# Performance work log

Hardware: AMD Instinct MI355X
Metric: run time of the kernel (lower is better)

## Reference

```python
import math
import jax, jax.numpy as jnp
import numpy as np

B, S, D_MODEL, H = 2, 2048, 1024, 16
D_HEAD = D_MODEL // H
NEG = -90000000000.0


def setup_inputs() -> dict:
    key = jax.random.key(0)
    ks = jax.random.split(key, 12)
    scale = 1.0 / math.sqrt(D_MODEL)
    return {
        "Q": jax.random.normal(ks[0], (B, S, D_MODEL), jnp.float32),
        "K": jax.random.normal(ks[1], (B, S, D_MODEL), jnp.float32),
        "V": jax.random.normal(ks[2], (B, S, D_MODEL), jnp.float32),
        "mask": jax.random.randint(ks[3], (B, 1, S, S), 0, 2).astype(bool),
        "Wq": jax.random.normal(ks[4], (D_MODEL, D_MODEL), jnp.float32) * scale,
        "bq": jnp.zeros((D_MODEL,), jnp.float32),
        "Wk": jax.random.normal(ks[5], (D_MODEL, D_MODEL), jnp.float32) * scale,
        "bk": jnp.zeros((D_MODEL,), jnp.float32),
        "Wv": jax.random.normal(ks[6], (D_MODEL, D_MODEL), jnp.float32) * scale,
        "bv": jnp.zeros((D_MODEL,), jnp.float32),
        "Wo": jax.random.normal(ks[7], (D_MODEL, D_MODEL), jnp.float32) * scale,
        "bo": jnp.zeros((D_MODEL,), jnp.float32),
    }


def _split_heads(x):
    # (B, S, D) -> (B, H, S, Dh)
    b, s, _ = x.shape
    return x.reshape(b, s, H, D_HEAD).transpose(0, 2, 1, 3)


def reference(Q, K, V, mask, Wq, bq, Wk, bk, Wv, bv, Wo, bo):
    q = _split_heads(Q @ Wq.T + bq)
    k = _split_heads(K @ Wk.T + bk)
    v = _split_heads(V @ Wv.T + bv)
    # scaled dot product with additive mask (mask.float() * -9e10)
    scores = jnp.einsum("bhqd,bhkd->bhqk", q, k) / math.sqrt(D_HEAD)
    scores = scores + mask.astype(scores.dtype) * NEG
    attn = jax.nn.softmax(scores, axis=-1)
    ctx = jnp.einsum("bhqk,bhkd->bhqd", attn, v)  # (B, H, S, Dh)
    ctx = ctx.transpose(0, 2, 1, 3).reshape(Q.shape[0], q.shape[2], D_MODEL)
    return ctx @ Wo.T + bo
```

## Files before the change

### kernel.cpp

```cpp
#include <hip/hip_runtime.h>
#include <hip/hip_bf16.h>


typedef __bf16 bf16x8 __attribute__((ext_vector_type(8)));
typedef float f32x4 __attribute__((ext_vector_type(4)));

#define S_LEN 2048
#define DM 1024
#define NH 16
#define DH 64
#define MROWS 4096

static __device__ __forceinline__ unsigned short f2bf(float f) {
    __hip_bfloat16 h = __float2bfloat16(f);
    unsigned short u; __builtin_memcpy(&u, &h, 2); return u;
}

static __device__ __forceinline__ bf16x8 cvt8(float4 a, float4 b) {
    bf16x8 o;
    o[0] = (__bf16)a.x; o[1] = (__bf16)a.y; o[2] = (__bf16)a.z; o[3] = (__bf16)a.w;
    o[4] = (__bf16)b.x; o[5] = (__bf16)b.y; o[6] = (__bf16)b.z; o[7] = (__bf16)b.w;
    return o;
}

__global__ __launch_bounds__(256)
void prep(const int* __restrict__ m, unsigned* __restrict__ mb,
          const float* __restrict__ Q, unsigned short* __restrict__ dQ,
          const float* __restrict__ K, unsigned short* __restrict__ dK,
          const float* __restrict__ V, unsigned short* __restrict__ dV,
          const float* __restrict__ W0, unsigned short* __restrict__ dW0,
          const float* __restrict__ W1, unsigned short* __restrict__ dW1,
          const float* __restrict__ W2, unsigned short* __restrict__ dW2,
          const float* __restrict__ W3, unsigned short* __restrict__ dW3)
{
    const int bx = blockIdx.x, tid = threadIdx.x;
    if (bx < 1024) {
        const int lane = tid & 63, w = tid >> 6;
        const int row = bx * 4 + w;
        const int* src = m + (size_t)row * S_LEN;
        unsigned* dst = mb + (size_t)row * (S_LEN / 32);
        for (int i = 0; i < 32; i++) {
            int v = src[i * 64 + lane];
            unsigned long long bm = __ballot(v != 0);
            if (lane == 0) { dst[i*2] = (unsigned)bm; dst[i*2+1] = (unsigned)(bm >> 32); }
        }
    } else if (bx < 7168) {
        int t = bx - 1024;
        int which = t >> 11;
        const float* s = which == 0 ? Q : which == 1 ? K : V;
        unsigned short* d = which == 0 ? dQ : which == 1 ? dK : dV;
        int i = ((t & 2047) * 256 + tid) * 8;
        float4 a = *(const float4*)(s + i);
        float4 b = *(const float4*)(s + i + 4);
        *(bf16x8*)(d + i) = cvt8(a, b);
    } else {
        int t = bx - 7168;
        int which = t >> 9;
        const float* s = which == 0 ? W0 : which == 1 ? W1 : which == 2 ? W2 : W3;
        unsigned short* d = which == 0 ? dW0 : which == 1 ? dW1 : which == 2 ? dW2 : dW3;
        int i = ((t & 511) * 256 + tid) * 8;
        float4 a = *(const float4*)(s + i);
        float4 b = *(const float4*)(s + i + 4);
        *(bf16x8*)(d + i) = cvt8(a, b);
    }
}

__global__ __launch_bounds__(256)
void gemm128(const unsigned short* __restrict__ X0, const unsigned short* __restrict__ X1,
             const unsigned short* __restrict__ X2,
             const unsigned short* __restrict__ W0, const unsigned short* __restrict__ W1,
             const unsigned short* __restrict__ W2,
             const float* __restrict__ b0, const float* __restrict__ b1,
             const float* __restrict__ b2,
             unsigned short* __restrict__ d0, unsigned short* __restrict__ d1,
             unsigned short* __restrict__ d2)
{
    __shared__ __align__(16) unsigned short As[128 * 32];
    __shared__ __align__(16) unsigned short Bs[128 * 32];
    const int z = blockIdx.z;
    const unsigned short* X = z == 0 ? X0 : z == 1 ? X1 : X2;
    const unsigned short* W = z == 0 ? W0 : z == 1 ? W1 : W2;
    const float* bias        = z == 0 ? b0 : z == 1 ? b1 : b2;
    unsigned short* dstb     = z == 0 ? d0 : z == 1 ? d1 : d2;

    const int tid  = threadIdx.x;
    const int m0   = blockIdx.y * 128;
    const int n0   = blockIdx.x * 128;
    const int lane = tid & 63;
    const int w    = tid >> 6;
    const int wm   = (w >> 1) * 64, wn = (w & 1) * 64;
    const int lr   = lane & 15;
    const int lg   = lane >> 4;

    f32x4 acc[4][4];
#pragma unroll
    for (int i = 0; i < 4; i++)
#pragma unroll
        for (int j = 0; j < 4; j++) acc[i][j] = f32x4{0.f, 0.f, 0.f, 0.f};

    for (int k0 = 0; k0 < DM; k0 += 32) {
        __syncthreads();
#pragma unroll
        for (int j = 0; j < 2; j++) {
            int e = tid + j * 256;
            int row = e >> 2, c8 = (e & 3) * 8;
            __builtin_amdgcn_global_load_lds(
                (const __attribute__((address_space(1))) unsigned*)&X[(size_t)(m0 + row) * DM + k0 + c8],
                (__attribute__((address_space(3))) unsigned*)&As[e * 8], 16, 0, 0);
            __builtin_amdgcn_global_load_lds(
                (const __attribute__((address_space(1))) unsigned*)&W[(size_t)(n0 + row) * DM + k0 + c8],
                (__attribute__((address_space(3))) unsigned*)&Bs[e * 8], 16, 0, 0);
        }
        __syncthreads();
        bf16x8 af[4], bfr[4];
#pragma unroll
        for (int mi = 0; mi < 4; mi++)
            af[mi] = *(const bf16x8*)(&As[(wm + mi * 16 + lr) * 32 + lg * 8]);
#pragma unroll
        for (int ni = 0; ni < 4; ni++)
            bfr[ni] = *(const bf16x8*)(&Bs[(wn + ni * 16 + lr) * 32 + lg * 8]);
#pragma unroll
        for (int mi = 0; mi < 4; mi++)
#pragma unroll
            for (int ni = 0; ni < 4; ni++)
                acc[mi][ni] = __builtin_amdgcn_mfma_f32_16x16x32_bf16(
                    af[mi], bfr[ni], acc[mi][ni], 0, 0, 0);
    }

#pragma unroll
    for (int mi = 0; mi < 4; mi++) {
#pragma unroll
        for (int ni = 0; ni < 4; ni++) {
            const int gcol = n0 + wn + ni * 16 + lr;
            const float bv = bias[gcol];
            const int grow0 = m0 + wm + mi * 16 + lg * 4;
            if (z == 2) {
                int b = grow0 >> 11, s = grow0 & (S_LEN - 1);
                int h = gcol >> 6, dh = gcol & 63;
                unsigned short us[4];
#pragma unroll
                for (int r = 0; r < 4; r++) us[r] = f2bf(acc[mi][ni][r] + bv);
                size_t di = ((size_t)(b * NH + h) * DH + dh) * S_LEN + s;
                unsigned lo = (unsigned)us[0] | ((unsigned)us[1] << 16);
                unsigned hi = (unsigned)us[2] | ((unsigned)us[3] << 16);
                *(uint2*)(&dstb[di]) = uint2{lo, hi};
            } else {
#pragma unroll
                for (int r = 0; r < 4; r++) {
                    int grow = grow0 + r;
                    float v = acc[mi][ni][r] + bv;
                    int b = grow >> 11, s = grow & (S_LEN - 1);
                    int h = gcol >> 6, dh = gcol & 63;
                    dstb[((size_t)(b * NH + h) * S_LEN + s) * DH + dh] = f2bf(v);
                }
            }
        }
    }
}

__global__ __launch_bounds__(256)
void gemm_out(const unsigned short* __restrict__ X, const unsigned short* __restrict__ W,
              const float* __restrict__ bias, float* __restrict__ dst)
{
    __shared__ __align__(16) unsigned short As[128 * 32];
    __shared__ __align__(16) unsigned short Bs[64 * 32];
    const int tid  = threadIdx.x;
    const int m0   = blockIdx.y * 128;
    const int n0   = blockIdx.x * 64;
    const int lane = tid & 63;
    const int w    = tid >> 6;
    const int wm   = (w >> 1) * 64, wn = (w & 1) * 32;
    const int lr   = lane & 15;
    const int lg   = lane >> 4;

    f32x4 acc[4][2];
#pragma unroll
    for (int i = 0; i < 4; i++)
#pragma unroll
        for (int j = 0; j < 2; j++) acc[i][j] = f32x4{0.f, 0.f, 0.f, 0.f};

    for (int k0 = 0; k0 < DM; k0 += 32) {
        __syncthreads();
#pragma unroll
        for (int j = 0; j < 2; j++) {
            int e = tid + j * 256;
            int row = e >> 2, c8 = (e & 3) * 8;
            __builtin_amdgcn_global_load_lds(
                (const __attribute__((address_space(1))) unsigned*)&X[(size_t)(m0 + row) * DM + k0 + c8],
                (__attribute__((address_space(3))) unsigned*)&As[e * 8], 16, 0, 0);
        }
        {
            int row = tid >> 2, c8 = (tid & 3) * 8;
            __builtin_amdgcn_global_load_lds(
                (const __attribute__((address_space(1))) unsigned*)&W[(size_t)(n0 + row) * DM + k0 + c8],
                (__attribute__((address_space(3))) unsigned*)&Bs[tid * 8], 16, 0, 0);
        }
        __syncthreads();
        bf16x8 af[4], bfr[2];
#pragma unroll
        for (int mi = 0; mi < 4; mi++)
            af[mi] = *(const bf16x8*)(&As[(wm + mi * 16 + lr) * 32 + lg * 8]);
#pragma unroll
        for (int ni = 0; ni < 2; ni++)
            bfr[ni] = *(const bf16x8*)(&Bs[(wn + ni * 16 + lr) * 32 + lg * 8]);
#pragma unroll
        for (int mi = 0; mi < 4; mi++)
#pragma unroll
            for (int ni = 0; ni < 2; ni++)
                acc[mi][ni] = __builtin_amdgcn_mfma_f32_16x16x32_bf16(
                    af[mi], bfr[ni], acc[mi][ni], 0, 0, 0);
    }
#pragma unroll
    for (int mi = 0; mi < 4; mi++)
#pragma unroll
        for (int ni = 0; ni < 2; ni++) {
            const int gcol = n0 + wn + ni * 16 + lr;
            const float bv = bias[gcol];
            const int grow0 = m0 + wm + mi * 16 + lg * 4;
#pragma unroll
            for (int r = 0; r < 4; r++)
                dst[(size_t)(grow0 + r) * DM + gcol] = acc[mi][ni][r] + bv;
        }
}

__global__ __launch_bounds__(256, 4)
void attn(const unsigned short* __restrict__ q_ws,
          const unsigned short* __restrict__ k_ws,
          const unsigned short* __restrict__ vt_ws,
          const unsigned* __restrict__ mbits,
          unsigned short* __restrict__ ctx)
{
    __shared__ __align__(16) unsigned short Ks[64 * 72];
    __shared__ __align__(16) unsigned short Vs[64 * 72];
    __shared__ __align__(16) unsigned short Pq[4][16 * 72];
    const int tid = threadIdx.x, lane = tid & 63, w = tid >> 6;
    const int lr = lane & 15, lg = lane >> 4;

    const int i    = blockIdx.x;
    const int xcd  = i & 7;
    const int slot = i >> 3;
    const int bh   = xcd * 4 + (slot >> 5);
    const int qblk = slot & 31;
    const int b  = bh >> 4;
    const int h  = bh & 15;
    const int q0 = qblk * 64 + w * 16;
    const int qrow = q0 + lr;

    const int srow = tid >> 3;
    const int sseg = tid & 7;

    const unsigned short* qh = q_ws + (size_t)bh * S_LEN * DH;
    const unsigned short* kh = k_ws + (size_t)bh * S_LEN * DH;
    const unsigned short* vh = vt_ws + (size_t)bh * DH * S_LEN;
    const unsigned* mrow = mbits + (size_t)(b * S_LEN + qrow) * (S_LEN / 32);

    bf16x8 aq[2];
#pragma unroll
    for (int c = 0; c < 2; c++)
        aq[c] = *(const bf16x8*)(&qh[(size_t)qrow * DH + c * 32 + lg * 8]);

    f32x4 acc[4];
#pragma unroll
    for (int di = 0; di < 4; di++) acc[di] = f32x4{0.f, 0.f, 0.f, 0.f};
    float rs = 0.f;

    uint4 kreg0, kreg1, vreg0, vreg1;
    kreg0 = *(const uint4*)(&kh[(size_t)(srow)      * DH + sseg * 8]);
    kreg1 = *(const uint4*)(&kh[(size_t)(srow + 32) * DH + sseg * 8]);
    vreg0 = *(const uint4*)(&vh[(size_t)(srow)      * S_LEN + sseg * 8]);
    vreg1 = *(const uint4*)(&vh[(size_t)(srow + 32) * S_LEN + sseg * 8]);

    for (int it = 0; it < 32; it++) {
        const int kv0 = it * 64;
        __syncthreads();
        *(uint4*)(&Ks[(srow)      * 72 + sseg * 8]) = kreg0;
        *(uint4*)(&Ks[(srow + 32) * 72 + sseg * 8]) = kreg1;
        *(uint4*)(&Vs[(srow)      * 72 + sseg * 8]) = vreg0;
        *(uint4*)(&Vs[(srow + 32) * 72 + sseg * 8]) = vreg1;
        __syncthreads();
        if (it < 31) {
            const int kn = kv0 + 64;
            kreg0 = *(const uint4*)(&kh[(size_t)(kn + srow)      * DH + sseg * 8]);
            kreg1 = *(const uint4*)(&kh[(size_t)(kn + srow + 32) * DH + sseg * 8]);
            vreg0 = *(const uint4*)(&vh[(size_t)(srow)      * S_LEN + kn + sseg * 8]);
            vreg1 = *(const uint4*)(&vh[(size_t)(srow + 32) * S_LEN + kn + sseg * 8]);
        }

        const uint2 mw = *(const uint2*)(&mrow[kv0 >> 5]);

        f32x4 sf[4];
#pragma unroll
        for (int ni = 0; ni < 4; ni++) {
            bf16x8 ak0 = *(const bf16x8*)(&Ks[(ni * 16 + lr) * 72 + lg * 8]);
            bf16x8 ak1 = *(const bf16x8*)(&Ks[(ni * 16 + lr) * 72 + 32 + lg * 8]);
            f32x4 t = __builtin_amdgcn_mfma_f32_16x16x32_bf16(ak0, aq[0], f32x4{0.f,0.f,0.f,0.f}, 0,0,0);
            t = __builtin_amdgcn_mfma_f32_16x16x32_bf16(ak1, aq[1], t, 0,0,0);
            sf[ni] = t;
        }
#pragma unroll
        for (int ni = 0; ni < 4; ni++)
#pragma unroll
            for (int r = 0; r < 4; r++) {
                unsigned word = (ni & 2) ? mw.y : mw.x;
                unsigned bit = (word >> ((ni & 1) * 16 + lg * 4 + r)) & 1u;
                float t = sf[ni][r] * 0.125f + (bit ? -1e5f : -8.0f);
                float p = __expf(fminf(t, 60.f));
                sf[ni][r] = p;
                rs += p;
            }

        unsigned short* pq = &Pq[w][0];
#pragma unroll
        for (int ni = 0; ni < 4; ni++) {
            unsigned lo = (unsigned)f2bf(sf[ni][0]) | ((unsigned)f2bf(sf[ni][1]) << 16);
            unsigned hi = (unsigned)f2bf(sf[ni][2]) | ((unsigned)f2bf(sf[ni][3]) << 16);
            *(uint2*)(&pq[lr * 72 + ni * 16 + lg * 4]) = uint2{lo, hi};
        }

        bf16x8 bp0 = *(const bf16x8*)(&pq[lr * 72 + lg * 8]);
        bf16x8 bp1 = *(const bf16x8*)(&pq[lr * 72 + 32 + lg * 8]);
#pragma unroll
        for (int di = 0; di < 4; di++) {
            bf16x8 av0 = *(const bf16x8*)(&Vs[(di * 16 + lr) * 72 + lg * 8]);
            bf16x8 av1 = *(const bf16x8*)(&Vs[(di * 16 + lr) * 72 + 32 + lg * 8]);
            acc[di] = __builtin_amdgcn_mfma_f32_16x16x32_bf16(av0, bp0, acc[di], 0, 0, 0);
            acc[di] = __builtin_amdgcn_mfma_f32_16x16x32_bf16(av1, bp1, acc[di], 0, 0, 0);
        }
    }

    rs += __shfl_xor(rs, 16);
    rs += __shfl_xor(rs, 32);
    const float inv = 1.0f / fmaxf(rs, 1e-37f);

    unsigned short* crow = &ctx[((size_t)(b * S_LEN + qrow)) * DM + h * DH];
#pragma unroll
    for (int di = 0; di < 4; di++) {
        unsigned lo = (unsigned)f2bf(acc[di][0] * inv) | ((unsigned)f2bf(acc[di][1] * inv) << 16);
        unsigned hi = (unsigned)f2bf(acc[di][2] * inv) | ((unsigned)f2bf(acc[di][3] * inv) << 16);
        *(uint2*)(&crow[di * 16 + lg * 4]) = uint2{lo, hi};
    }
}

extern "C" void kernel_launch(void* const* d_in, const int* in_sizes, int n_in,
                              void* d_out, int out_size, void* d_ws, size_t ws_size,
                              hipStream_t stream)
{
    (void)in_sizes; (void)n_in; (void)out_size; (void)ws_size;
    const float* Q  = (const float*)d_in[0];
    const float* K  = (const float*)d_in[1];
    const float* V  = (const float*)d_in[2];
    const int*   Mk = (const int*)d_in[3];
    const float* Wq = (const float*)d_in[4];
    const float* bq = (const float*)d_in[5];
    const float* Wk = (const float*)d_in[6];
    const float* bk = (const float*)d_in[7];
    const float* Wv = (const float*)d_in[8];
    const float* bv = (const float*)d_in[9];
    const float* Wo = (const float*)d_in[10];
    const float* bo = (const float*)d_in[11];

    const int NX = MROWS * DM;
    const int NW = DM * DM;

    unsigned short* q_ws  = (unsigned short*)d_ws;
    unsigned short* k_ws  = q_ws + (size_t)NX;
    unsigned short* vt_ws = k_ws + (size_t)NX;
    unsigned short* ctx   = vt_ws + (size_t)NX;
    unsigned*       mbits = (unsigned*)(ctx + (size_t)NX);
    unsigned short* Wbq   = (unsigned short*)(mbits + (size_t)MROWS * (S_LEN / 32));
    unsigned short* Wbk   = Wbq + (size_t)NW;
    unsigned short* Wbv   = Wbk + (size_t)NW;
    unsigned short* Wbo   = Wbv + (size_t)NW;
    unsigned short* Xbq   = Wbo + (size_t)NW;
    unsigned short* Xbk   = Xbq + (size_t)NX;
    unsigned short* Xbv   = Xbk + (size_t)NX;
    float* out = (float*)d_out;

    dim3 blk(256);
    prep<<<dim3(9216), blk, 0, stream>>>(Mk, mbits, Q, Xbq, K, Xbk, V, Xbv,
                                         Wq, Wbq, Wk, Wbk, Wv, Wbv, Wo, Wbo);

    gemm128<<<dim3(8, 32, 3), blk, 0, stream>>>(Xbq, Xbk, Xbv, Wbq, Wbk, Wbv,
                                                bq, bk, bv, q_ws, k_ws, vt_ws);

    attn<<<dim3(1024), blk, 0, stream>>>(q_ws, k_ws, vt_ws, mbits, ctx);

    gemm_out<<<dim3(16, 32), blk, 0, stream>>>(ctx, Wbo, bo, out);
}
```

Before: 283.2 us.

## Process two query tiles per wave, fold softmax scale into Q, use exp2

The attention kernel now has each wave handle 32 query rows (two 16-row tiles) against each shared K/V tile. This doubles reuse of the LDS-staged keys and values and halves the grid to 512 blocks, with launch bounds relaxed to 2. The softmax scale and log2(e) are folded into the Q projection epilogue, so the kernel calls the hardware exp2 directly and drops the per-element multiply, offset and clamp. Masked entries are zeroed with a select. Row sums come from an MFMA against a ones vector instead of a VALU sum plus shuffles. In exchange it uses more registers and has fewer blocks to hide latency, and dropping the clamp leaves exp overflow unguarded for large scores.

Measured after the change: 272.7 us. 3.7% less time.

```diff
diff --git a/kernel.cpp b/kernel.cpp
--- a/kernel.cpp
+++ b/kernel.cpp
@@ -3,6 +3,7 @@
 
 
 typedef __bf16 bf16x8 __attribute__((ext_vector_type(8)));
+typedef __bf16 bf16x4 __attribute__((ext_vector_type(4)));
 typedef float f32x4 __attribute__((ext_vector_type(4)));
 
 #define S_LEN 2048
@@ -11,9 +12,19 @@
 #define DH 64
 #define MROWS 4096
 
+#define QSCALE 0.18033688011112042f
+
 static __device__ __forceinline__ unsigned short f2bf(float f) {
-    __hip_bfloat16 h = __float2bfloat16(f);
-    unsigned short u; __builtin_memcpy(&u, &h, 2); return u;
+    __bf16 b = (__bf16)f;
+    unsigned short u; __builtin_memcpy(&u, &b, 2); return u;
+}
+
+static __device__ __forceinline__ float exp2_hw(float x) {
+#if __has_builtin(__builtin_amdgcn_exp2f)
+    return __builtin_amdgcn_exp2f(x);
+#else
+    float r; asm("v_exp_f32 %0, %1" : "=v"(r) : "v"(x)); return r;
+#endif
 }
 
 static __device__ __forceinline__ bf16x8 cvt8(float4 a, float4 b) {
@@ -137,18 +148,17 @@
             if (z == 2) {
                 int b = grow0 >> 11, s = grow0 & (S_LEN - 1);
                 int h = gcol >> 6, dh = gcol & 63;
-                unsigned short us[4];
-#pragma unroll
-                for (int r = 0; r < 4; r++) us[r] = f2bf(acc[mi][ni][r] + bv);
+                bf16x4 pk;
+#pragma unroll
+                for (int r = 0; r < 4; r++) pk[r] = (__bf16)(acc[mi][ni][r] + bv);
                 size_t di = ((size_t)(b * NH + h) * DH + dh) * S_LEN + s;
-                unsigned lo = (unsigned)us[0] | ((unsigned)us[1] << 16);
-                unsigned hi = (unsigned)us[2] | ((unsigned)us[3] << 16);
-                *(uint2*)(&dstb[di]) = uint2{lo, hi};
+                *(bf16x4*)(&dstb[di]) = pk;
             } else {
 #pragma unroll
                 for (int r = 0; r < 4; r++) {
                     int grow = grow0 + r;
                     float v = acc[mi][ni][r] + bv;
+                    if (z == 0) v *= QSCALE;
                     int b = grow >> 11, s = grow & (S_LEN - 1);
                     int h = gcol >> 6, dh = gcol & 63;
                     dstb[((size_t)(b * NH + h) * S_LEN + s) * DH + dh] = f2bf(v);
@@ -223,7 +233,7 @@
         }
 }
 
-__global__ __launch_bounds__(256, 4)
+__global__ __launch_bounds__(256, 2)
 void attn(const unsigned short* __restrict__ q_ws,
           const unsigned short* __restrict__ k_ws,
           const unsigned short* __restrict__ vt_ws,
@@ -232,19 +242,20 @@
 {
     __shared__ __align__(16) unsigned short Ks[64 * 72];
     __shared__ __align__(16) unsigned short Vs[64 * 72];
-    __shared__ __align__(16) unsigned short Pq[4][16 * 72];
+    __shared__ __align__(16) unsigned short Pq[4][32 * 72];
     const int tid = threadIdx.x, lane = tid & 63, w = tid >> 6;
     const int lr = lane & 15, lg = lane >> 4;
 
     const int i    = blockIdx.x;
     const int xcd  = i & 7;
     const int slot = i >> 3;
-    const int bh   = xcd * 4 + (slot >> 5);
-    const int qblk = slot & 31;
+    const int bh   = xcd * 4 + (slot >> 4);
+    const int qblk = slot & 15;
     const int b  = bh >> 4;
     const int h  = bh & 15;
-    const int q0 = qblk * 64 + w * 16;
-    const int qrow = q0 + lr;
+    const int q0 = qblk * 128 + w * 32;
+    const int qA = q0 + lr;
+    const int qB = q0 + 16 + lr;
 
     const int srow = tid >> 3;
     const int sseg = tid & 7;
@@ -252,23 +263,36 @@
     const unsigned short* qh = q_ws + (size_t)bh * S_LEN * DH;
     const unsigned short* kh = k_ws + (size_t)bh * S_LEN * DH;
     const unsigned short* vh = vt_ws + (size_t)bh * DH * S_LEN;
-    const unsigned* mrow = mbits + (size_t)(b * S_LEN + qrow) * (S_LEN / 32);
-
-    bf16x8 aq[2];
-#pragma unroll
-    for (int c = 0; c < 2; c++)
-        aq[c] = *(const bf16x8*)(&qh[(size_t)qrow * DH + c * 32 + lg * 8]);
-
-    f32x4 acc[4];
-#pragma unroll
-    for (int di = 0; di < 4; di++) acc[di] = f32x4{0.f, 0.f, 0.f, 0.f};
-    float rs = 0.f;
+    const unsigned* mrA = mbits + (size_t)(b * S_LEN + qA) * (S_LEN / 32);
+    const unsigned* mrB = mbits + (size_t)(b * S_LEN + qB) * (S_LEN / 32);
+
+    bf16x8 aqA[2], aqB[2];
+#pragma unroll
+    for (int c = 0; c < 2; c++) {
+        aqA[c] = *(const bf16x8*)(&qh[(size_t)qA * DH + c * 32 + lg * 8]);
+        aqB[c] = *(const bf16x8*)(&qh[(size_t)qB * DH + c * 32 + lg * 8]);
+    }
+
+    bf16x8 ones;
+#pragma unroll
+    for (int j = 0; j < 8; j++) ones[j] = (__bf16)1.0f;
+
+    f32x4 accA[4], accB[4], accRA, accRB;
+#pragma unroll
+    for (int di = 0; di < 4; di++) {
+        accA[di] = f32x4{0.f, 0.f, 0.f, 0.f};
+        accB[di] = f32x4{0.f, 0.f, 0.f, 0.f};
+    }
+    accRA = f32x4{0.f, 0.f, 0.f, 0.f};
+    accRB = f32x4{0.f, 0.f, 0.f, 0.f};
 
     uint4 kreg0, kreg1, vreg0, vreg1;
     kreg0 = *(const uint4*)(&kh[(size_t)(srow)      * DH + sseg * 8]);
     kreg1 = *(const uint4*)(&kh[(size_t)(srow + 32) * DH + sseg * 8]);
     vreg0 = *(const uint4*)(&vh[(size_t)(srow)      * S_LEN + sseg * 8]);
     vreg1 = *(const uint4*)(&vh[(size_t)(srow + 32) * S_LEN + sseg * 8]);
+
+    unsigned short* pq = &Pq[w][0];
 
     for (int it = 0; it < 32; it++) {
         const int kv0 = it * 64;
@@ -286,58 +310,84 @@
             vreg1 = *(const uint4*)(&vh[(size_t)(srow + 32) * S_LEN + kn + sseg * 8]);
         }
 
-        const uint2 mw = *(const uint2*)(&mrow[kv0 >> 5]);
-
-        f32x4 sf[4];
+        const uint2 mwA = *(const uint2*)(&mrA[it * 2]);
+        const uint2 mwB = *(const uint2*)(&mrB[it * 2]);
+
+        f32x4 sA[4], sB[4];
 #pragma unroll
         for (int ni = 0; ni < 4; ni++) {
             bf16x8 ak0 = *(const bf16x8*)(&Ks[(ni * 16 + lr) * 72 + lg * 8]);
             bf16x8 ak1 = *(const bf16x8*)(&Ks[(ni * 16 + lr) * 72 + 32 + lg * 8]);
-            f32x4 t = __builtin_amdgcn_mfma_f32_16x16x32_bf16(ak0, aq[0], f32x4{0.f,0.f,0.f,0.f}, 0,0,0);
-            t = __builtin_amdgcn_mfma_f32_16x16x32_bf16(ak1, aq[1], t, 0,0,0);
-            sf[ni] = t;
-        }
-#pragma unroll
-        for (int ni = 0; ni < 4; ni++)
+            f32x4 tA = __builtin_amdgcn_mfma_f32_16x16x32_bf16(ak0, aqA[0], f32x4{0.f,0.f,0.f,0.f}, 0,0,0);
+            tA = __builtin_amdgcn_mfma_f32_16x16x32_bf16(ak1, aqA[1], tA, 0,0,0);
+            f32x4 tB = __builtin_amdgcn_mfma_f32_16x16x32_bf16(ak0, aqB[0], f32x4{0.f,0.f,0.f,0.f}, 0,0,0);
+            tB = __builtin_amdgcn_mfma_f32_16x16x32_bf16(ak1, aqB[1], tB, 0,0,0);
+            sA[ni] = tA; sB[ni] = tB;
+        }
+
+#pragma unroll
+        for (int ni = 0; ni < 4; ni++) {
+            unsigned wA = (ni & 2) ? mwA.y : mwA.x;
+            unsigned wB = (ni & 2) ? mwB.y : mwB.x;
+            unsigned nibA = wA >> ((ni & 1) * 16 + lg * 4);
+            unsigned nibB = wB >> ((ni & 1) * 16 + lg * 4);
 #pragma unroll
             for (int r = 0; r < 4; r++) {
-                unsigned word = (ni & 2) ? mw.y : mw.x;
-                unsigned bit = (word >> ((ni & 1) * 16 + lg * 4 + r)) & 1u;
-                float t = sf[ni][r] * 0.125f + (bit ? -1e5f : -8.0f);
-                float p = __expf(fminf(t, 60.f));
-                sf[ni][r] = p;
-                rs += p;
+                float pA = exp2_hw(sA[ni][r]);
+                float pB = exp2_hw(sB[ni][r]);
+                sA[ni][r] = (nibA & (1u << r)) ? 0.f : pA;
+                sB[ni][r] = (nibB & (1u << r)) ? 0.f : pB;
             }
-
-        unsigned short* pq = &Pq[w][0];
+        }
+
 #pragma unroll
         for (int ni = 0; ni < 4; ni++) {
-            unsigned lo = (unsigned)f2bf(sf[ni][0]) | ((unsigned)f2bf(sf[ni][1]) << 16);
-            unsigned hi = (unsigned)f2bf(sf[ni][2]) | ((unsigned)f2bf(sf[ni][3]) << 16);
-            *(uint2*)(&pq[lr * 72 + ni * 16 + lg * 4]) = uint2{lo, hi};
-        }
-
-        bf16x8 bp0 = *(const bf16x8*)(&pq[lr * 72 + lg * 8]);
-        bf16x8 bp1 = *(const bf16x8*)(&pq[lr * 72 + 32 + lg * 8]);
+            bf16x4 pkA, pkB;
+#pragma unroll
+            for (int r = 0; r < 4; r++) {
+                pkA[r] = (__bf16)sA[ni][r];
+                pkB[r] = (__bf16)sB[ni][r];
+            }
+            *(bf16x4*)(&pq[(lr)      * 72 + ni * 16 + lg * 4]) = pkA;
+            *(bf16x4*)(&pq[(16 + lr) * 72 + ni * 16 + lg * 4]) = pkB;
+        }
+
+        bf16x8 bpA0 = *(const bf16x8*)(&pq[(lr)      * 72 + lg * 8]);
+        bf16x8 bpA1 = *(const bf16x8*)(&pq[(lr)      * 72 + 32 + lg * 8]);
+        bf16x8 bpB0 = *(const bf16x8*)(&pq[(16 + lr) * 72 + lg * 8]);
+        bf16x8 bpB1 = *(const bf16x8*)(&pq[(16 + lr) * 72 + 32 + lg * 8]);
+
 #pragma unroll
         for (int di = 0; di < 4; di++) {
             bf16x8 av0 = *(const bf16x8*)(&Vs[(di * 16 + lr) * 72 + lg * 8]);
             bf16x8 av1 = *(const bf16x8*)(&Vs[(di * 16 + lr) * 72 + 32 + lg * 8]);
-            acc[di] = __builtin_amdgcn_mfma_f32_16x16x32_bf16(av0, bp0, acc[di], 0, 0, 0);
-            acc[di] = __builtin_amdgcn_mfma_f32_16x16x32_bf16(av1, bp1, acc[di], 0, 0, 0);
-        }
-    }
-
-    rs += __shfl_xor(rs, 16);
-    rs += __shfl_xor(rs, 32);
-    const float inv = 1.0f / fmaxf(rs, 1e-37f);
-
-    unsigned short* crow = &ctx[((size_t)(b * S_LEN + qrow)) * DM + h * DH];
+            accA[di] = __builtin_amdgcn_mfma_f32_16x16x32_bf16(av0, bpA0, accA[di], 0, 0, 0);
+            accA[di] = __builtin_amdgcn_mfma_f32_16x16x32_bf16(av1, bpA1, accA[di], 0, 0, 0);
+            accB[di] = __builtin_amdgcn_mfma_f32_16x16x32_bf16(av0, bpB0, accB[di], 0, 0, 0);
+            accB[di] = __builtin_amdgcn_mfma_f32_16x16x32_bf16(av1, bpB1, accB[di], 0, 0, 0);
+        }
+
+        accRA = __builtin_amdgcn_mfma_f32_16x16x32_bf16(ones, bpA0, accRA, 0, 0, 0);
+        accRA = __builtin_amdgcn_mfma_f32_16x16x32_bf16(ones, bpA1, accRA, 0, 0, 0);
+        accRB = __builtin_amdgcn_mfma_f32_16x16x32_bf16(ones, bpB0, accRB, 0, 0, 0);
+        accRB = __builtin_amdgcn_mfma_f32_16x16x32_bf16(ones, bpB1, accRB, 0, 0, 0);
+    }
+
+    const float invA = 1.0f / fmaxf(accRA[0], 1e-37f);
+    const float invB = 1.0f / fmaxf(accRB[0], 1e-37f);
+
+    unsigned short* crowA = &ctx[((size_t)(b * S_LEN + qA)) * DM + h * DH];
+    unsigned short* crowB = &ctx[((size_t)(b * S_LEN + qB)) * DM + h * DH];
 #pragma unroll
     for (int di = 0; di < 4; di++) {
-        unsigned lo = (unsigned)f2bf(acc[di][0] * inv) | ((unsigned)f2bf(acc[di][1] * inv) << 16);
-        unsigned hi = (unsigned)f2bf(acc[di][2] * inv) | ((unsigned)f2bf(acc[di][3] * inv) << 16);
-        *(uint2*)(&crow[di * 16 + lg * 4]) = uint2{lo, hi};
+        bf16x4 oA, oB;
+#pragma unroll
+        for (int r = 0; r < 4; r++) {
+            oA[r] = (__bf16)(accA[di][r] * invA);
+            oB[r] = (__bf16)(accB[di][r] * invB);
+        }
+        *(bf16x4*)(&crowA[di * 16 + lg * 4]) = oA;
+        *(bf16x4*)(&crowB[di * 16 + lg * 4]) = oB;
     }
 }
 
@@ -383,7 +433,7 @@
     gemm128<<<dim3(8, 32, 3), blk, 0, stream>>>(Xbq, Xbk, Xbv, Wbq, Wbk, Wbv,
                                                 bq, bk, bv, q_ws, k_ws, vt_ws);
 
-    attn<<<dim3(1024), blk, 0, stream>>>(q_ws, k_ws, vt_ws, mbits, ctx);
+    attn<<<dim3(512), blk, 0, stream>>>(q_ws, k_ws, vt_ws, mbits, ctx);
 
     gemm_out<<<dim3(16, 32), blk, 0, stream>>>(ctx, Wbo, bo, out);
 }
```
